# Performance work log

Hardware: AMD Instinct MI355X
Metric: run time of the kernel (lower is better)

## Reference

```python
import jax, jax.numpy as jnp
import numpy as np

N = 65536          # number of input vectors
D = 128            # embedding_dim
K = 2048           # num_embeddings (codebook size)
DH = D // 2        # linear_proj output dim


def setup_inputs() -> dict:
    key = jax.random.key(0)
    k1, k2, k3, k4 = jax.random.split(key, 4)
    z = jax.random.normal(k1, (N, D), dtype=jnp.float32)
    # linear_proj params (nn.Linear(D, D//2)): weight [DH, D], bias [DH]
    W = jax.random.normal(k2, (DH, D), dtype=jnp.float32) * (1.0 / np.sqrt(D))
    b = jax.random.normal(k3, (DH,), dtype=jnp.float32) * 0.01
    # codebook buffer, initialized ~ N(0,1) as in the torch module
    embeddings = jax.random.normal(k4, (K, D), dtype=jnp.float32)
    return {"z": z, "W": W, "b": b, "embeddings": embeddings}


def reference(z, W, b, embeddings):
    # project inputs and codebook into half-dim space
    z_ = z @ W.T + b                       # [N, DH]
    emb_ = embeddings @ W.T + b            # [K, DH]
    # squared euclidean distances via ||a||^2 + ||b||^2 - 2 a.b
    distances = ((z_ ** 2).sum(-1, keepdims=True)
                 + (emb_ ** 2).sum(-1)
                 - 2.0 * (z_ @ emb_.T))    # [N, K]
    closest = jnp.argmin(distances, axis=-1)               # [N]
    one_hot_encoding = jax.nn.one_hot(closest, K, dtype=jnp.float32)  # [N, K]
    quantized = one_hot_encoding @ embeddings               # [N, D] (gather)
    return (quantized, one_hot_encoding)
```

## Files before the change

kernel.cpp:

```cpp
#include <hip/hip_runtime.h>
#include <float.h>

#define N_ROWS 65536
#define D_IN   128
#define DH     64
#define K_CB   2048

typedef const __attribute__((address_space(1))) void* gas_p;
typedef __attribute__((address_space(3))) void* las_p;
typedef _Float16 f16x8 __attribute__((ext_vector_type(8)));
typedef float    f32x4 __attribute__((ext_vector_type(4)));

__global__ __launch_bounds__(256) void k_project(
    const float* __restrict__ Z, const float* __restrict__ emb,
    const float* __restrict__ W, const float* __restrict__ b,
    _Float16* __restrict__ zpl,
    _Float16* __restrict__ epl,
    float* __restrict__ e2,
    float* __restrict__ outOH) {
  __shared__ __align__(16) float Wl[64 * 140];
  __shared__ __align__(16) float Zl[16 * 128];
  int tid = threadIdx.x;
  const float* src; _Float16* dst; int n0; bool do_e2; size_t plane;
  if ((int)blockIdx.x < 4096) {
    src = Z;   dst = zpl; n0 = blockIdx.x * 16;          do_e2 = false; plane = (size_t)N_ROWS * 64;
  } else {
    src = emb; dst = epl; n0 = (blockIdx.x - 4096) * 16; do_e2 = true;  plane = (size_t)K_CB * 64;
  }

#pragma unroll
  for (int i = 0; i < 8; ++i) {
    int idx4 = tid + 256 * i;
    int j = idx4 >> 5;
    int d4 = (idx4 & 31) * 4;
    *(float4*)&Wl[j * 140 + d4] = *(const float4*)(W + j * 128 + d4);
  }
#pragma unroll
  for (int i = 0; i < 2; ++i) {
    int idx4 = tid + 256 * i;
    int r = idx4 >> 5;
    int d4 = (idx4 & 31) * 4;
    *(float4*)&Zl[r * 128 + d4] = *(const float4*)(src + (size_t)(n0 + r) * 128 + d4);
  }
  int j = tid & 63, g = tid >> 6;
  float bj = b[j];
  __syncthreads();

  if (outOH && (int)blockIdx.x < 4096) {
    f32x4 zz4 = (f32x4){0.f, 0.f, 0.f, 0.f};
    f32x4* dz = (f32x4*)(outOH + (size_t)n0 * K_CB);
#pragma unroll
    for (int i = 0; i < 32; ++i)
      __builtin_nontemporal_store(zz4, dz + tid + 256 * i);
  }

  float acc[4] = {0.f, 0.f, 0.f, 0.f};
  for (int d4 = 0; d4 < 128; d4 += 4) {
    float4 w4 = *(float4*)&Wl[j * 140 + d4];
#pragma unroll
    for (int i = 0; i < 4; ++i) {
      float4 z4 = *(float4*)&Zl[(g * 4 + i) * 128 + d4];
      acc[i] = fmaf(z4.x, w4.x, fmaf(z4.y, w4.y, fmaf(z4.z, w4.z, fmaf(z4.w, w4.w, acc[i]))));
    }
  }
#pragma unroll
  for (int i = 0; i < 4; ++i) {
    int n = n0 + g * 4 + i;
    float v = acc[i] + bj;
    _Float16 h = (_Float16)v;  float rm = v - (float)h;
    _Float16 m = (_Float16)rm;
    int pos = (((j >> 3) ^ (n & 7)) << 3) | (j & 7);
    size_t base = (size_t)n * 64 + pos;
    dst[base]         = h;
    dst[plane + base] = m;
    if (do_e2) {
      float s = v * v;
#pragma unroll
      for (int off = 32; off > 0; off >>= 1) s += __shfl_xor(s, off, 64);
      if (j == 0) e2[n] = s;
    }
  }
}

__global__ __launch_bounds__(256, 3) void k_score(
    const _Float16* __restrict__ zpl,
    const _Float16* __restrict__ epl,
    const float* __restrict__ e2,
    const float* __restrict__ emb,
    float* __restrict__ outQ,
    float* __restrict__ outOH,
    int* __restrict__ cidx_g) {
  __shared__ __align__(16) char U[49152];
  _Float16* Zs  = (_Float16*)U;
  char*     es0 = U + 16384;
  char*     es1 = U + 32768;

  int tid = threadIdx.x, lane = tid & 63, wid = tid >> 6;
  int quad = lane >> 4, l16 = lane & 15;
  int row0 = blockIdx.x * 64;

  for (int q = wid; q < 16; q += 4) {
    int p = q >> 3, within = (q & 7) * 1024;
    const char* g = (const char*)zpl + (size_t)p * ((size_t)N_ROWS * 128)
                  + (size_t)row0 * 128 + within + lane * 16;
    __builtin_amdgcn_global_load_lds((gas_p)g, (las_p)((char*)Zs + p * 8192 + within), 16, 0, 0);
  }
  for (int q = wid; q < 16; q += 4) {
    int p = q >> 3, within = (q & 7) * 1024;
    const char* g = (const char*)epl + (size_t)p * (K_CB * 128) + within + lane * 16;
    __builtin_amdgcn_global_load_lds((gas_p)g, (las_p)(es0 + p * 8192 + within), 16, 0, 0);
  }

  __syncthreads();

  f16x8 A[2][4][2];
#pragma unroll
  for (int step = 0; step < 2; ++step)
#pragma unroll
    for (int mt = 0; mt < 4; ++mt) {
      int tr = mt * 16 + l16;
      int cph = (step * 4 + quad) ^ (tr & 7);
      const _Float16* pa = Zs + tr * 64 + cph * 8;
      A[step][mt][0] = *(const f16x8*)pa;
      A[step][mt][1] = *(const f16x8*)(pa + 4096);
    }

  float best[16]; int bidx[16];
#pragma unroll
  for (int s = 0; s < 16; ++s) { best[s] = FLT_MAX; bidx[s] = 0; }

  for (int t = 0; t < 32; ++t) {
    const _Float16* esc = (const _Float16*)((t & 1) ? es1 : es0);
    if (t < 31) {
      char* esn = (t & 1) ? es0 : es1;
      for (int q = wid; q < 16; q += 4) {
        int p = q >> 3, within = (q & 7) * 1024;
        const char* g = (const char*)epl + (size_t)p * (K_CB * 128)
                      + (size_t)(t + 1) * 8192 + within + lane * 16;
        __builtin_amdgcn_global_load_lds((gas_p)g, (las_p)(esn + p * 8192 + within), 16, 0, 0);
      }
    }
    int col = t * 64 + wid * 16 + l16;
    float ev = e2[col];

    f32x4 accf[4];
#pragma unroll
    for (int mt = 0; mt < 4; ++mt) accf[mt] = (f32x4){0.f, 0.f, 0.f, 0.f};

#pragma unroll
    for (int step = 0; step < 2; ++step) {
      int tc = wid * 16 + l16;
      int cph = (step * 4 + quad) ^ (l16 & 7);
      const _Float16* pb = esc + tc * 64 + cph * 8;
      f16x8 Bh = *(const f16x8*)pb;
      f16x8 Bm = *(const f16x8*)(pb + 4096);
#pragma unroll
      for (int mt = 0; mt < 4; ++mt) {
        f32x4 c = accf[mt];
        c = __builtin_amdgcn_mfma_f32_16x16x32_f16(A[step][mt][1], Bm, c, 0, 0, 0);
        c = __builtin_amdgcn_mfma_f32_16x16x32_f16(A[step][mt][1], Bh, c, 0, 0, 0);
        c = __builtin_amdgcn_mfma_f32_16x16x32_f16(A[step][mt][0], Bm, c, 0, 0, 0);
        c = __builtin_amdgcn_mfma_f32_16x16x32_f16(A[step][mt][0], Bh, c, 0, 0, 0);
        accf[mt] = c;
      }
    }

#pragma unroll
    for (int mt = 0; mt < 4; ++mt)
#pragma unroll
      for (int r = 0; r < 4; ++r) {
        float s = fmaf(-2.0f, accf[mt][r], ev);
        int slot = mt * 4 + r;
        if (s < best[slot]) { best[slot] = s; bidx[slot] = col; }
      }

    __syncthreads();
  }

  float* redm = (float*)U;
  int*   redi = (int*)(U + 16384);
#pragma unroll
  for (int mt = 0; mt < 4; ++mt)
#pragma unroll
    for (int r = 0; r < 4; ++r) {
      int row = mt * 16 + quad * 4 + r;
      redm[row * 64 + wid * 16 + l16] = best[mt * 4 + r];
      redi[row * 64 + wid * 16 + l16] = bidx[mt * 4 + r];
    }
  __syncthreads();
  int* cidx = (int*)(U + 32768);
  if (tid < 64) {
    float m = redm[tid * 64]; int mi = redi[tid * 64];
    for (int s = 1; s < 64; ++s) {
      float v = redm[tid * 64 + s]; int vi = redi[tid * 64 + s];
      if (v < m || (v == m && vi < mi)) { m = v; mi = vi; }
    }
    cidx[tid] = mi;
  }
  __syncthreads();

  if (outOH) {
    if (tid < 64) outOH[(size_t)(row0 + tid) * K_CB + cidx[tid]] = 1.0f;
  } else {
    if (tid < 64) cidx_g[row0 + tid] = cidx[tid];
  }

#pragma unroll
  for (int i = 0; i < 8; ++i) {
    int idx = tid + 256 * i;
    int r = idx >> 5, c = (idx & 31) * 4;
    f32x4 v = *(const f32x4*)(emb + (size_t)cidx[r] * D_IN + c);
    __builtin_nontemporal_store(v, (f32x4*)(outQ + (size_t)(row0 + r) * D_IN + c));
  }
}

__global__ void k_epilogue(const int* __restrict__ cidx_g, float* __restrict__ outOH) {
  int tid  = threadIdx.x;
  int row0 = blockIdx.x * 64;
  float4 zz4 = make_float4(0.f, 0.f, 0.f, 0.f);
  for (int r = 0; r < 64; ++r) {
    float4* dst = (float4*)(outOH + (size_t)(row0 + r) * K_CB);
    dst[tid]       = zz4;
    dst[tid + 256] = zz4;
  }
  __syncthreads();
  if (tid < 64) {
    int r = row0 + tid;
    outOH[(size_t)r * K_CB + cidx_g[r]] = 1.0f;
  }
}

extern "C" void kernel_launch(void* const* d_in, const int* in_sizes, int n_in,
                              void* d_out, int out_size, void* d_ws, size_t ws_size,
                              hipStream_t stream) {
  (void)in_sizes; (void)n_in; (void)out_size;
  const float* Z   = (const float*)d_in[0];
  const float* W   = (const float*)d_in[1];
  const float* b   = (const float*)d_in[2];
  const float* emb = (const float*)d_in[3];
  float* outQ  = (float*)d_out;
  float* outOH = (float*)d_out + (size_t)N_ROWS * D_IN;

  char* wsb = (char*)d_ws;
  _Float16* epl = (_Float16*)wsb;
  float*    e2  = (float*)(wsb + 524288);
  const size_t need_primary = 524288 + 8192 + (size_t)2 * N_ROWS * 64 * 2;

  if (ws_size >= need_primary) {
    _Float16* zpl = (_Float16*)(wsb + 532480);
    k_project<<<4224, 256, 0, stream>>>(Z, emb, W, b, zpl, epl, e2, outOH);
    k_score<<<1024, 256, 0, stream>>>(zpl, epl, e2, emb, outQ, outOH, nullptr);
  } else {
    int*      cidx_g = (int*)(wsb + 532480);
    _Float16* zpl    = (_Float16*)outOH;
    k_project<<<4224, 256, 0, stream>>>(Z, emb, W, b, zpl, epl, e2, nullptr);
    k_score<<<1024, 256, 0, stream>>>(zpl, epl, e2, emb, outQ, nullptr, cidx_g);
    k_epilogue<<<1024, 256, 0, stream>>>(cidx_g, outOH);
  }
}
```

Baseline: 676.4 us.

## Fuse Z projection into scoring kernel with MFMA and triple-buffered codebook

Moves the Z projection out of a separate kernel and into the scoring kernel. Each block loads raw Z rows into LDS and projects them with split-f16 MFMAs against a W fragment buffer prepared once. This drops the write and reread of the projected Z planes in global memory. The codebook tiles are now triple-buffered with explicit vmcnt waits and a single barrier per step, and the one-hot zeroing stores are interleaved into the scoring loop. In exchange, occupancy drops to 2 blocks per SIMD and the hand-counted waits add some risk.

Measured after the change: 871.5 us. +28.8%, slower.

```diff
diff --git a/kernel.cpp b/kernel.cpp
--- a/kernel.cpp
+++ b/kernel.cpp
@@ -11,22 +11,31 @@
 typedef _Float16 f16x8 __attribute__((ext_vector_type(8)));
 typedef float    f32x4 __attribute__((ext_vector_type(4)));
 
-__global__ __launch_bounds__(256) void k_project(
-    const float* __restrict__ Z, const float* __restrict__ emb,
-    const float* __restrict__ W, const float* __restrict__ b,
-    _Float16* __restrict__ zpl,
+__global__ __launch_bounds__(256) void k_prep(
+    const float* __restrict__ emb, const float* __restrict__ W,
+    const float* __restrict__ b,
     _Float16* __restrict__ epl,
     float* __restrict__ e2,
-    float* __restrict__ outOH) {
+    _Float16* __restrict__ wfrag) {
+  int tid = threadIdx.x;
+  if (blockIdx.x == 128) {
+    for (int g = tid; g < 8192; g += 256) {
+      int e = g & 7, lane = (g >> 3) & 63, nt = (g >> 9) & 3, ks = (g >> 11) & 3;
+      int k = ks * 32 + (lane >> 4) * 8 + e;
+      int j = nt * 16 + (lane & 15);
+      float v = W[j * 128 + k];
+      _Float16 h = (_Float16)v;
+      _Float16 m = (_Float16)(v - (float)h);
+      int idx = ((ks * 4 + nt) * 64 + lane) * 8 + e;
+      wfrag[idx]        = h;
+      wfrag[8192 + idx] = m;
+    }
+    return;
+  }
   __shared__ __align__(16) float Wl[64 * 140];
   __shared__ __align__(16) float Zl[16 * 128];
-  int tid = threadIdx.x;
-  const float* src; _Float16* dst; int n0; bool do_e2; size_t plane;
-  if ((int)blockIdx.x < 4096) {
-    src = Z;   dst = zpl; n0 = blockIdx.x * 16;          do_e2 = false; plane = (size_t)N_ROWS * 64;
-  } else {
-    src = emb; dst = epl; n0 = (blockIdx.x - 4096) * 16; do_e2 = true;  plane = (size_t)K_CB * 64;
-  }
+  int n0 = blockIdx.x * 16;
+  const size_t plane = (size_t)K_CB * 64;
 
 #pragma unroll
   for (int i = 0; i < 8; ++i) {
@@ -40,19 +49,11 @@
     int idx4 = tid + 256 * i;
     int r = idx4 >> 5;
     int d4 = (idx4 & 31) * 4;
-    *(float4*)&Zl[r * 128 + d4] = *(const float4*)(src + (size_t)(n0 + r) * 128 + d4);
+    *(float4*)&Zl[r * 128 + d4] = *(const float4*)(emb + (size_t)(n0 + r) * 128 + d4);
   }
   int j = tid & 63, g = tid >> 6;
   float bj = b[j];
   __syncthreads();
-
-  if (outOH && (int)blockIdx.x < 4096) {
-    f32x4 zz4 = (f32x4){0.f, 0.f, 0.f, 0.f};
-    f32x4* dz = (f32x4*)(outOH + (size_t)n0 * K_CB);
-#pragma unroll
-    for (int i = 0; i < 32; ++i)
-      __builtin_nontemporal_store(zz4, dz + tid + 256 * i);
-  }
 
   float acc[4] = {0.f, 0.f, 0.f, 0.f};
   for (int d4 = 0; d4 < 128; d4 += 4) {
@@ -71,46 +72,94 @@
     _Float16 m = (_Float16)rm;
     int pos = (((j >> 3) ^ (n & 7)) << 3) | (j & 7);
     size_t base = (size_t)n * 64 + pos;
-    dst[base]         = h;
-    dst[plane + base] = m;
-    if (do_e2) {
-      float s = v * v;
-#pragma unroll
-      for (int off = 32; off > 0; off >>= 1) s += __shfl_xor(s, off, 64);
-      if (j == 0) e2[n] = s;
-    }
+    epl[base]         = h;
+    epl[plane + base] = m;
+    float s = v * v;
+#pragma unroll
+    for (int off = 32; off > 0; off >>= 1) s += __shfl_xor(s, off, 64);
+    if (j == 0) e2[n] = s;
   }
 }
 
-__global__ __launch_bounds__(256, 3) void k_score(
-    const _Float16* __restrict__ zpl,
+__global__ __launch_bounds__(256, 2) void k_main(
+    const float* __restrict__ Z,
+    const float* __restrict__ b,
     const _Float16* __restrict__ epl,
+    const _Float16* __restrict__ wfrag,
     const float* __restrict__ e2,
     const float* __restrict__ emb,
     float* __restrict__ outQ,
-    float* __restrict__ outOH,
-    int* __restrict__ cidx_g) {
+    float* __restrict__ outOH) {
   __shared__ __align__(16) char U[49152];
-  _Float16* Zs  = (_Float16*)U;
-  char*     es0 = U + 16384;
-  char*     es1 = U + 32768;
-
   int tid = threadIdx.x, lane = tid & 63, wid = tid >> 6;
   int quad = lane >> 4, l16 = lane & 15;
   int row0 = blockIdx.x * 64;
 
-  for (int q = wid; q < 16; q += 4) {
-    int p = q >> 3, within = (q & 7) * 1024;
-    const char* g = (const char*)zpl + (size_t)p * ((size_t)N_ROWS * 128)
-                  + (size_t)row0 * 128 + within + lane * 16;
-    __builtin_amdgcn_global_load_lds((gas_p)g, (las_p)((char*)Zs + p * 8192 + within), 16, 0, 0);
-  }
-  for (int q = wid; q < 16; q += 4) {
-    int p = q >> 3, within = (q & 7) * 1024;
-    const char* g = (const char*)epl + (size_t)p * (K_CB * 128) + within + lane * 16;
-    __builtin_amdgcn_global_load_lds((gas_p)g, (las_p)(es0 + p * 8192 + within), 16, 0, 0);
-  }
-
+  for (int q2 = wid; q2 < 32; q2 += 4) {
+    int L = q2 * 1024 + lane * 16;
+    int r = L >> 9;
+    int pslot = (L >> 4) & 31;
+    const char* g = (const char*)(Z + (size_t)(row0 + r) * 128) + ((pslot ^ (r & 7)) * 16);
+    __builtin_amdgcn_global_load_lds((gas_p)g, (las_p)(U + q2 * 1024), 16, 0, 0);
+  }
+
+  float e2r[32];
+#pragma unroll
+  for (int t = 0; t < 32; ++t) e2r[t] = e2[t * 64 + wid * 16 + l16];
+  float bjr[4];
+#pragma unroll
+  for (int nt = 0; nt < 4; ++nt) bjr[nt] = b[nt * 16 + l16];
+
+  __syncthreads();
+
+  const float* Zraw = (const float*)U;
+  const f16x8* wf = (const f16x8*)wfrag;
+  f32x4 pacc[4];
+#pragma unroll
+  for (int nt = 0; nt < 4; ++nt) pacc[nt] = (f32x4){0.f, 0.f, 0.f, 0.f};
+  int zrow = wid * 16 + l16;
+#pragma unroll
+  for (int ks = 0; ks < 4; ++ks) {
+    int c0 = ks * 8 + quad * 2;
+    f32x4 v0 = *(const f32x4*)(Zraw + zrow * 128 + ((c0 ^ (zrow & 7)) * 4));
+    f32x4 v1 = *(const f32x4*)(Zraw + zrow * 128 + (((c0 + 1) ^ (zrow & 7)) * 4));
+    f16x8 Ah, Am;
+#pragma unroll
+    for (int e = 0; e < 4; ++e) {
+      _Float16 h0 = (_Float16)v0[e];
+      Ah[e] = h0;  Am[e] = (_Float16)(v0[e] - (float)h0);
+      _Float16 h1 = (_Float16)v1[e];
+      Ah[e + 4] = h1;  Am[e + 4] = (_Float16)(v1[e] - (float)h1);
+    }
+#pragma unroll
+    for (int nt = 0; nt < 4; ++nt) {
+      f16x8 Bh = wf[(ks * 4 + nt) * 64 + lane];
+      f16x8 Bm = wf[1024 + (ks * 4 + nt) * 64 + lane];
+      f32x4 c = pacc[nt];
+      c = __builtin_amdgcn_mfma_f32_16x16x32_f16(Am, Bm, c, 0, 0, 0);
+      c = __builtin_amdgcn_mfma_f32_16x16x32_f16(Am, Bh, c, 0, 0, 0);
+      c = __builtin_amdgcn_mfma_f32_16x16x32_f16(Ah, Bm, c, 0, 0, 0);
+      c = __builtin_amdgcn_mfma_f32_16x16x32_f16(Ah, Bh, c, 0, 0, 0);
+      pacc[nt] = c;
+    }
+  }
+  __syncthreads();
+
+  _Float16* Zs = (_Float16*)U;
+#pragma unroll
+  for (int nt = 0; nt < 4; ++nt) {
+    int j = nt * 16 + l16;
+#pragma unroll
+    for (int r = 0; r < 4; ++r) {
+      int row = wid * 16 + quad * 4 + r;
+      float v = pacc[nt][r] + bjr[nt];
+      _Float16 h = (_Float16)v;
+      _Float16 m = (_Float16)(v - (float)h);
+      int pos = (((j >> 3) ^ (row & 7)) << 3) | (j & 7);
+      Zs[row * 64 + pos]        = h;
+      Zs[4096 + row * 64 + pos] = m;
+    }
+  }
   __syncthreads();
 
   f16x8 A[2][4][2];
@@ -124,15 +173,23 @@
       A[step][mt][0] = *(const f16x8*)pa;
       A[step][mt][1] = *(const f16x8*)(pa + 4096);
     }
+  __syncthreads();
+
+  for (int q = wid; q < 16; q += 4) {
+    int p = q >> 3, within = (q & 7) * 1024;
+    const char* g = (const char*)epl + (size_t)p * (K_CB * 128) + within + lane * 16;
+    __builtin_amdgcn_global_load_lds((gas_p)g, (las_p)(U + p * 8192 + within), 16, 0, 0);
+  }
 
   float best[16]; int bidx[16];
 #pragma unroll
   for (int s = 0; s < 16; ++s) { best[s] = FLT_MAX; bidx[s] = 0; }
-
+  float* ohbase = outOH + (size_t)row0 * K_CB;
+
+#pragma unroll
   for (int t = 0; t < 32; ++t) {
-    const _Float16* esc = (const _Float16*)((t & 1) ? es1 : es0);
     if (t < 31) {
-      char* esn = (t & 1) ? es0 : es1;
+      char* esn = U + ((t + 1) % 3) * 16384;
       for (int q = wid; q < 16; q += 4) {
         int p = q >> 3, within = (q & 7) * 1024;
         const char* g = (const char*)epl + (size_t)p * (K_CB * 128)
@@ -140,9 +197,19 @@
         __builtin_amdgcn_global_load_lds((gas_p)g, (las_p)(esn + p * 8192 + within), 16, 0, 0);
       }
     }
-    int col = t * 64 + wid * 16 + l16;
-    float ev = e2[col];
-
+    {
+      f32x4 zz = (f32x4){0.f, 0.f, 0.f, 0.f};
+#pragma unroll
+      for (int s = 0; s < 4; ++s)
+        __builtin_nontemporal_store(zz, (f32x4*)(ohbase + t * 4096) + tid + 256 * s);
+    }
+    if (t < 31) { asm volatile("s_waitcnt vmcnt(8)" ::: "memory"); }
+    else        { asm volatile("s_waitcnt vmcnt(4)" ::: "memory"); }
+    __builtin_amdgcn_sched_barrier(0);
+    __builtin_amdgcn_s_barrier();
+    __builtin_amdgcn_sched_barrier(0);
+
+    const _Float16* esc = (const _Float16*)(U + (t % 3) * 16384);
     f32x4 accf[4];
 #pragma unroll
     for (int mt = 0; mt < 4; ++mt) accf[mt] = (f32x4){0.f, 0.f, 0.f, 0.f};
@@ -165,6 +232,8 @@
       }
     }
 
+    int col = t * 64 + wid * 16 + l16;
+    float ev = e2r[t];
 #pragma unroll
     for (int mt = 0; mt < 4; ++mt)
 #pragma unroll
@@ -173,9 +242,8 @@
         int slot = mt * 4 + r;
         if (s < best[slot]) { best[slot] = s; bidx[slot] = col; }
       }
-
-    __syncthreads();
-  }
+  }
+  __syncthreads();
 
   float* redm = (float*)U;
   int*   redi = (int*)(U + 16384);
@@ -199,11 +267,7 @@
   }
   __syncthreads();
 
-  if (outOH) {
-    if (tid < 64) outOH[(size_t)(row0 + tid) * K_CB + cidx[tid]] = 1.0f;
-  } else {
-    if (tid < 64) cidx_g[row0 + tid] = cidx[tid];
-  }
+  if (tid < 64) outOH[(size_t)(row0 + tid) * K_CB + cidx[tid]] = 1.0f;
 
 #pragma unroll
   for (int i = 0; i < 8; ++i) {
@@ -214,26 +278,10 @@
   }
 }
 
-__global__ void k_epilogue(const int* __restrict__ cidx_g, float* __restrict__ outOH) {
-  int tid  = threadIdx.x;
-  int row0 = blockIdx.x * 64;
-  float4 zz4 = make_float4(0.f, 0.f, 0.f, 0.f);
-  for (int r = 0; r < 64; ++r) {
-    float4* dst = (float4*)(outOH + (size_t)(row0 + r) * K_CB);
-    dst[tid]       = zz4;
-    dst[tid + 256] = zz4;
-  }
-  __syncthreads();
-  if (tid < 64) {
-    int r = row0 + tid;
-    outOH[(size_t)r * K_CB + cidx_g[r]] = 1.0f;
-  }
-}
-
 extern "C" void kernel_launch(void* const* d_in, const int* in_sizes, int n_in,
                               void* d_out, int out_size, void* d_ws, size_t ws_size,
                               hipStream_t stream) {
-  (void)in_sizes; (void)n_in; (void)out_size;
+  (void)in_sizes; (void)n_in; (void)out_size; (void)ws_size;
   const float* Z   = (const float*)d_in[0];
   const float* W   = (const float*)d_in[1];
   const float* b   = (const float*)d_in[2];
@@ -242,19 +290,10 @@
   float* outOH = (float*)d_out + (size_t)N_ROWS * D_IN;
 
   char* wsb = (char*)d_ws;
-  _Float16* epl = (_Float16*)wsb;
-  float*    e2  = (float*)(wsb + 524288);
-  const size_t need_primary = 524288 + 8192 + (size_t)2 * N_ROWS * 64 * 2;
-
-  if (ws_size >= need_primary) {
-    _Float16* zpl = (_Float16*)(wsb + 532480);
-    k_project<<<4224, 256, 0, stream>>>(Z, emb, W, b, zpl, epl, e2, outOH);
-    k_score<<<1024, 256, 0, stream>>>(zpl, epl, e2, emb, outQ, outOH, nullptr);
-  } else {
-    int*      cidx_g = (int*)(wsb + 532480);
-    _Float16* zpl    = (_Float16*)outOH;
-    k_project<<<4224, 256, 0, stream>>>(Z, emb, W, b, zpl, epl, e2, nullptr);
-    k_score<<<1024, 256, 0, stream>>>(zpl, epl, e2, emb, outQ, nullptr, cidx_g);
-    k_epilogue<<<1024, 256, 0, stream>>>(cidx_g, outOH);
-  }
+  _Float16* epl   = (_Float16*)wsb;
+  float*    e2    = (float*)(wsb + 524288);
+  _Float16* wfrag = (_Float16*)(wsb + 532480);
+
+  k_prep<<<129, 256, 0, stream>>>(emb, W, b, epl, e2, wfrag);
+  k_main<<<1024, 256, 0, stream>>>(Z, b, epl, wfrag, e2, emb, outQ, outOH);
 }
```

## Project 64 rows per block reading Z directly and interleave one-hot zeroing

Applied to the files above, without the earlier changes.

The projection kernel now handles 64 rows per block instead of 16, cutting the block count by four and amortizing the per-block load of W into shared memory. Z rows are read straight from global memory as broadcast float4 loads, so the shared staging buffer and its sync are gone. Each thread accumulates 16 rows. The zero-fill of the one-hot output is split into chunks between compute phases to overlap stores with math. Risks are higher register pressure, fewer blocks for latency hiding, and uncoalesced wave-uniform global loads of Z.

After: 2.162 ms. 220% more time.

```diff
diff --git a/kernel.cpp b/kernel.cpp
--- a/kernel.cpp
+++ b/kernel.cpp
@@ -19,13 +19,13 @@
     float* __restrict__ e2,
     float* __restrict__ outOH) {
   __shared__ __align__(16) float Wl[64 * 140];
-  __shared__ __align__(16) float Zl[16 * 128];
-  int tid = threadIdx.x;
-  const float* src; _Float16* dst; int n0; bool do_e2; size_t plane;
-  if ((int)blockIdx.x < 4096) {
-    src = Z;   dst = zpl; n0 = blockIdx.x * 16;          do_e2 = false; plane = (size_t)N_ROWS * 64;
+  int tid = threadIdx.x, lane = tid & 63, g = tid >> 6;
+  bool is_z = (int)blockIdx.x < 1024;
+  const float* src; _Float16* dst; int n0; size_t plane;
+  if (is_z) {
+    src = Z;   dst = zpl; n0 = blockIdx.x * 64;          plane = (size_t)N_ROWS * 64;
   } else {
-    src = emb; dst = epl; n0 = (blockIdx.x - 4096) * 16; do_e2 = true;  plane = (size_t)K_CB * 64;
+    src = emb; dst = epl; n0 = ((int)blockIdx.x - 1024) * 64; plane = (size_t)K_CB * 64;
   }
 
 #pragma unroll
@@ -35,49 +35,51 @@
     int d4 = (idx4 & 31) * 4;
     *(float4*)&Wl[j * 140 + d4] = *(const float4*)(W + j * 128 + d4);
   }
-#pragma unroll
-  for (int i = 0; i < 2; ++i) {
-    int idx4 = tid + 256 * i;
-    int r = idx4 >> 5;
-    int d4 = (idx4 & 31) * 4;
-    *(float4*)&Zl[r * 128 + d4] = *(const float4*)(src + (size_t)(n0 + r) * 128 + d4);
-  }
-  int j = tid & 63, g = tid >> 6;
-  float bj = b[j];
-  __syncthreads();
-
-  if (outOH && (int)blockIdx.x < 4096) {
-    f32x4 zz4 = (f32x4){0.f, 0.f, 0.f, 0.f};
-    f32x4* dz = (f32x4*)(outOH + (size_t)n0 * K_CB);
-#pragma unroll
-    for (int i = 0; i < 32; ++i)
-      __builtin_nontemporal_store(zz4, dz + tid + 256 * i);
-  }
-
-  float acc[4] = {0.f, 0.f, 0.f, 0.f};
-  for (int d4 = 0; d4 < 128; d4 += 4) {
-    float4 w4 = *(float4*)&Wl[j * 140 + d4];
-#pragma unroll
-    for (int i = 0; i < 4; ++i) {
-      float4 z4 = *(float4*)&Zl[(g * 4 + i) * 128 + d4];
-      acc[i] = fmaf(z4.x, w4.x, fmaf(z4.y, w4.y, fmaf(z4.z, w4.z, fmaf(z4.w, w4.w, acc[i]))));
-    }
-  }
-#pragma unroll
-  for (int i = 0; i < 4; ++i) {
-    int n = n0 + g * 4 + i;
+  float bj = b[lane];
+  __syncthreads();
+
+  const float* zbase = src + (size_t)(n0 + g * 16) * 128;
+  f32x4* ohrow = (is_z && outOH) ? (f32x4*)(outOH + (size_t)n0 * K_CB) : nullptr;
+
+  float acc[16];
+#pragma unroll
+  for (int i = 0; i < 16; ++i) acc[i] = 0.f;
+
+#pragma unroll
+  for (int c = 0; c < 4; ++c) {
+    if (ohrow) {
+      f32x4 zz = (f32x4){0.f, 0.f, 0.f, 0.f};
+#pragma unroll
+      for (int s2 = 0; s2 < 32; ++s2)
+        __builtin_nontemporal_store(zz, ohrow + c * 8192 + tid + 256 * s2);
+    }
+#pragma unroll
+    for (int dd = 0; dd < 8; ++dd) {
+      int d4 = c * 32 + dd * 4;
+      float4 w4 = *(float4*)&Wl[lane * 140 + d4];
+#pragma unroll
+      for (int i = 0; i < 16; ++i) {
+        float4 z4 = *(const float4*)(zbase + i * 128 + d4);
+        acc[i] = fmaf(z4.x, w4.x, fmaf(z4.y, w4.y, fmaf(z4.z, w4.z, fmaf(z4.w, w4.w, acc[i]))));
+      }
+    }
+  }
+
+#pragma unroll
+  for (int i = 0; i < 16; ++i) {
+    int n = n0 + g * 16 + i;
     float v = acc[i] + bj;
     _Float16 h = (_Float16)v;  float rm = v - (float)h;
     _Float16 m = (_Float16)rm;
-    int pos = (((j >> 3) ^ (n & 7)) << 3) | (j & 7);
+    int pos = (((lane >> 3) ^ (n & 7)) << 3) | (lane & 7);
     size_t base = (size_t)n * 64 + pos;
     dst[base]         = h;
     dst[plane + base] = m;
-    if (do_e2) {
+    if (!is_z) {
       float s = v * v;
 #pragma unroll
       for (int off = 32; off > 0; off >>= 1) s += __shfl_xor(s, off, 64);
-      if (j == 0) e2[n] = s;
+      if (lane == 0) e2[n] = s;
     }
   }
 }
@@ -248,12 +250,12 @@
 
   if (ws_size >= need_primary) {
     _Float16* zpl = (_Float16*)(wsb + 532480);
-    k_project<<<4224, 256, 0, stream>>>(Z, emb, W, b, zpl, epl, e2, outOH);
+    k_project<<<1056, 256, 0, stream>>>(Z, emb, W, b, zpl, epl, e2, outOH);
     k_score<<<1024, 256, 0, stream>>>(zpl, epl, e2, emb, outQ, outOH, nullptr);
   } else {
     int*      cidx_g = (int*)(wsb + 532480);
     _Float16* zpl    = (_Float16*)outOH;
-    k_project<<<4224, 256, 0, stream>>>(Z, emb, W, b, zpl, epl, e2, nullptr);
+    k_project<<<1056, 256, 0, stream>>>(Z, emb, W, b, zpl, epl, e2, nullptr);
     k_score<<<1024, 256, 0, stream>>>(zpl, epl, e2, emb, outQ, nullptr, cidx_g);
     k_epilogue<<<1024, 256, 0, stream>>>(cidx_g, outOH);
   }
```

## Double score-kernel row tile to 128 rows per block to reuse codebook tiles

Applied to the files above, without the earlier changes.

Each k_score block now handles 128 input rows instead of 64, halving the grid to 512 blocks. The first 64 rows keep their A fragments in registers, while the second 64 rows are reloaded from LDS on every step. The goal is to halve the number of times the codebook tiles are streamed from global memory into LDS per row, cutting load and sync overhead relative to MFMA work. In exchange, LDS use grows to 64KB, occupancy drops to 2 blocks per CU, and the extra LDS reads for the second row group add latency.

New measurement: 664.6 us. Within noise of the previous version (-1.8%).

```diff
diff --git a/kernel.cpp b/kernel.cpp
--- a/kernel.cpp
+++ b/kernel.cpp
@@ -82,7 +82,7 @@
   }
 }
 
-__global__ __launch_bounds__(256, 3) void k_score(
+__global__ __launch_bounds__(256, 2) void k_score(
     const _Float16* __restrict__ zpl,
     const _Float16* __restrict__ epl,
     const float* __restrict__ e2,
@@ -90,20 +90,21 @@
     float* __restrict__ outQ,
     float* __restrict__ outOH,
     int* __restrict__ cidx_g) {
-  __shared__ __align__(16) char U[49152];
+  __shared__ __align__(16) char U[65536];
   _Float16* Zs  = (_Float16*)U;
-  char*     es0 = U + 16384;
-  char*     es1 = U + 32768;
+  char*     es0 = U + 32768;
+  char*     es1 = U + 49152;
+  __shared__ int cidxs[128];
 
   int tid = threadIdx.x, lane = tid & 63, wid = tid >> 6;
   int quad = lane >> 4, l16 = lane & 15;
-  int row0 = blockIdx.x * 64;
-
-  for (int q = wid; q < 16; q += 4) {
-    int p = q >> 3, within = (q & 7) * 1024;
+  int row0 = blockIdx.x * 128;
+
+  for (int q = wid; q < 32; q += 4) {
+    int p = q >> 4, within = (q & 15) * 1024;
     const char* g = (const char*)zpl + (size_t)p * ((size_t)N_ROWS * 128)
                   + (size_t)row0 * 128 + within + lane * 16;
-    __builtin_amdgcn_global_load_lds((gas_p)g, (las_p)((char*)Zs + p * 8192 + within), 16, 0, 0);
+    __builtin_amdgcn_global_load_lds((gas_p)g, (las_p)((char*)Zs + p * 16384 + within), 16, 0, 0);
   }
   for (int q = wid; q < 16; q += 4) {
     int p = q >> 3, within = (q & 7) * 1024;
@@ -122,12 +123,12 @@
       int cph = (step * 4 + quad) ^ (tr & 7);
       const _Float16* pa = Zs + tr * 64 + cph * 8;
       A[step][mt][0] = *(const f16x8*)pa;
-      A[step][mt][1] = *(const f16x8*)(pa + 4096);
-    }
-
-  float best[16]; int bidx[16];
-#pragma unroll
-  for (int s = 0; s < 16; ++s) { best[s] = FLT_MAX; bidx[s] = 0; }
+      A[step][mt][1] = *(const f16x8*)(pa + 8192);
+    }
+
+  float best[32]; int bidx[32];
+#pragma unroll
+  for (int s = 0; s < 32; ++s) { best[s] = FLT_MAX; bidx[s] = 0; }
 
   for (int t = 0; t < 32; ++t) {
     const _Float16* esc = (const _Float16*)((t & 1) ? es1 : es0);
@@ -143,9 +144,12 @@
     int col = t * 64 + wid * 16 + l16;
     float ev = e2[col];
 
-    f32x4 accf[4];
-#pragma unroll
-    for (int mt = 0; mt < 4; ++mt) accf[mt] = (f32x4){0.f, 0.f, 0.f, 0.f};
+    f32x4 acc0[4], acc1[4];
+#pragma unroll
+    for (int mt = 0; mt < 4; ++mt) {
+      acc0[mt] = (f32x4){0.f, 0.f, 0.f, 0.f};
+      acc1[mt] = (f32x4){0.f, 0.f, 0.f, 0.f};
+    }
 
 #pragma unroll
     for (int step = 0; step < 2; ++step) {
@@ -156,12 +160,26 @@
       f16x8 Bm = *(const f16x8*)(pb + 4096);
 #pragma unroll
       for (int mt = 0; mt < 4; ++mt) {
-        f32x4 c = accf[mt];
+        f32x4 c = acc0[mt];
         c = __builtin_amdgcn_mfma_f32_16x16x32_f16(A[step][mt][1], Bm, c, 0, 0, 0);
         c = __builtin_amdgcn_mfma_f32_16x16x32_f16(A[step][mt][1], Bh, c, 0, 0, 0);
         c = __builtin_amdgcn_mfma_f32_16x16x32_f16(A[step][mt][0], Bm, c, 0, 0, 0);
         c = __builtin_amdgcn_mfma_f32_16x16x32_f16(A[step][mt][0], Bh, c, 0, 0, 0);
-        accf[mt] = c;
+        acc0[mt] = c;
+      }
+#pragma unroll
+      for (int mt = 0; mt < 4; ++mt) {
+        int tr = 64 + mt * 16 + l16;
+        int cph1 = (step * 4 + quad) ^ (tr & 7);
+        const _Float16* pa = Zs + tr * 64 + cph1 * 8;
+        f16x8 Ah = *(const f16x8*)pa;
+        f16x8 Am = *(const f16x8*)(pa + 8192);
+        f32x4 c = acc1[mt];
+        c = __builtin_amdgcn_mfma_f32_16x16x32_f16(Am, Bm, c, 0, 0, 0);
+        c = __builtin_amdgcn_mfma_f32_16x16x32_f16(Am, Bh, c, 0, 0, 0);
+        c = __builtin_amdgcn_mfma_f32_16x16x32_f16(Ah, Bm, c, 0, 0, 0);
+        c = __builtin_amdgcn_mfma_f32_16x16x32_f16(Ah, Bh, c, 0, 0, 0);
+        acc1[mt] = c;
       }
     }
 
@@ -169,47 +187,50 @@
     for (int mt = 0; mt < 4; ++mt)
 #pragma unroll
       for (int r = 0; r < 4; ++r) {
-        float s = fmaf(-2.0f, accf[mt][r], ev);
+        float s0 = fmaf(-2.0f, acc0[mt][r], ev);
         int slot = mt * 4 + r;
-        if (s < best[slot]) { best[slot] = s; bidx[slot] = col; }
+        if (s0 < best[slot]) { best[slot] = s0; bidx[slot] = col; }
+        float s1 = fmaf(-2.0f, acc1[mt][r], ev);
+        if (s1 < best[16 + slot]) { best[16 + slot] = s1; bidx[16 + slot] = col; }
       }
 
     __syncthreads();
   }
 
   float* redm = (float*)U;
-  int*   redi = (int*)(U + 16384);
-#pragma unroll
-  for (int mt = 0; mt < 4; ++mt)
-#pragma unroll
-    for (int r = 0; r < 4; ++r) {
-      int row = mt * 16 + quad * 4 + r;
-      redm[row * 64 + wid * 16 + l16] = best[mt * 4 + r];
-      redi[row * 64 + wid * 16 + l16] = bidx[mt * 4 + r];
-    }
-  __syncthreads();
-  int* cidx = (int*)(U + 32768);
-  if (tid < 64) {
+  int*   redi = (int*)(U + 32768);
+#pragma unroll
+  for (int grp = 0; grp < 2; ++grp)
+#pragma unroll
+    for (int mt = 0; mt < 4; ++mt)
+#pragma unroll
+      for (int r = 0; r < 4; ++r) {
+        int row = grp * 64 + mt * 16 + quad * 4 + r;
+        redm[row * 64 + wid * 16 + l16] = best[grp * 16 + mt * 4 + r];
+        redi[row * 64 + wid * 16 + l16] = bidx[grp * 16 + mt * 4 + r];
+      }
+  __syncthreads();
+  if (tid < 128) {
     float m = redm[tid * 64]; int mi = redi[tid * 64];
     for (int s = 1; s < 64; ++s) {
       float v = redm[tid * 64 + s]; int vi = redi[tid * 64 + s];
       if (v < m || (v == m && vi < mi)) { m = v; mi = vi; }
     }
-    cidx[tid] = mi;
+    cidxs[tid] = mi;
   }
   __syncthreads();
 
   if (outOH) {
-    if (tid < 64) outOH[(size_t)(row0 + tid) * K_CB + cidx[tid]] = 1.0f;
+    if (tid < 128) outOH[(size_t)(row0 + tid) * K_CB + cidxs[tid]] = 1.0f;
   } else {
-    if (tid < 64) cidx_g[row0 + tid] = cidx[tid];
-  }
-
-#pragma unroll
-  for (int i = 0; i < 8; ++i) {
+    if (tid < 128) cidx_g[row0 + tid] = cidxs[tid];
+  }
+
+#pragma unroll
+  for (int i = 0; i < 16; ++i) {
     int idx = tid + 256 * i;
     int r = idx >> 5, c = (idx & 31) * 4;
-    f32x4 v = *(const f32x4*)(emb + (size_t)cidx[r] * D_IN + c);
+    f32x4 v = *(const f32x4*)(emb + (size_t)cidxs[r] * D_IN + c);
     __builtin_nontemporal_store(v, (f32x4*)(outQ + (size_t)(row0 + r) * D_IN + c));
   }
 }
@@ -249,12 +270,12 @@
   if (ws_size >= need_primary) {
     _Float16* zpl = (_Float16*)(wsb + 532480);
     k_project<<<4224, 256, 0, stream>>>(Z, emb, W, b, zpl, epl, e2, outOH);
-    k_score<<<1024, 256, 0, stream>>>(zpl, epl, e2, emb, outQ, outOH, nullptr);
+    k_score<<<512, 256, 0, stream>>>(zpl, epl, e2, emb, outQ, outOH, nullptr);
   } else {
     int*      cidx_g = (int*)(wsb + 532480);
     _Float16* zpl    = (_Float16*)outOH;
     k_project<<<4224, 256, 0, stream>>>(Z, emb, W, b, zpl, epl, e2, nullptr);
-    k_score<<<1024, 256, 0, stream>>>(zpl, epl, e2, emb, outQ, nullptr, cidx_g);
+    k_score<<<512, 256, 0, stream>>>(zpl, epl, e2, emb, outQ, nullptr, cidx_g);
     k_epilogue<<<1024, 256, 0, stream>>>(cidx_g, outOH);
   }
 }
```
